# Optimization experiments

Measured on AMD Instinct MI355X. Metric: run time of the kernel, lower is better.

The kernel has to match this reference:

```python
import jax, jax.numpy as jnp
import numpy as np

B, LQ, LK, DIM = 2, 2048, 2048, 1024
HEADS, DH = 8, 64
INNER = HEADS * DH  # 512


def setup_inputs() -> dict:
    key = jax.random.key(0)
    ks = jax.random.split(key, 7)
    x = jax.random.normal(ks[0], (B, LQ, DIM), dtype=jnp.float32)
    y = jax.random.normal(ks[1], (B, LK, DIM), dtype=jnp.float32)
    # binary mask, 1 => masked (gets -1e9 added)
    mask = jax.random.randint(ks[2], (B, LQ, LK), 0, 2).astype(jnp.float32)
    s = 0.02
    Wq = jax.random.normal(ks[3], (INNER, DIM), dtype=jnp.float32) * s
    Wk = jax.random.normal(ks[4], (INNER, DIM), dtype=jnp.float32) * s
    Wv = jax.random.normal(ks[5], (INNER, DIM), dtype=jnp.float32) * s
    Wo = jax.random.normal(ks[6], (DIM, INNER), dtype=jnp.float32) * s
    return {"x": x, "y": y, "mask": mask, "Wq": Wq, "Wk": Wk, "Wv": Wv, "Wo": Wo}


def reference(x, y, mask, Wq, Wk, Wv, Wo):
    scale = DH ** -0.5
    # projections (Linear without bias: x @ W.T)
    q = (x @ Wq.T) * scale            # [B, LQ, INNER]
    k = y @ Wk.T                      # [B, LK, INNER]
    v = y @ Wv.T                      # [B, LK, INNER]
    # split into heads (torch.split along last dim == reshape to [.., H, DH])
    q = q.reshape(B, LQ, HEADS, DH)
    k = k.reshape(B, LK, HEADS, DH)
    v = v.reshape(B, LK, HEADS, DH)
    # per-head QK^T + additive mask*-1e9, softmax over keys, then V
    scores = jnp.einsum('bqhd,bkhd->bhqk', q, k) + mask[:, None, :, :] * (-1e9)
    attn = jax.nn.softmax(scores, axis=-1)
    out = jnp.einsum('bhqk,bkhd->bqhd', attn, v).reshape(B, LQ, INNER)
    return out @ Wo.T                 # [B, LQ, DIM]
```

## Files before the change

### kernel.cpp

```cpp
#include <hip/hip_runtime.h>
#include <hip/hip_bf16.h>
#include <stdint.h>

#define BATCH 2
#define LQ 2048
#define LK 2048
#define DIM 1024
#define HEADS 8
#define DH 64
#define INNER 512

typedef __attribute__((ext_vector_type(8))) short short8;
typedef __attribute__((ext_vector_type(4))) float f32x4;

__device__ __forceinline__ float bf2f(unsigned short u) {
    union { unsigned int i; float f; } v;
    v.i = ((unsigned int)u) << 16;
    return v.f;
}
__device__ __forceinline__ unsigned short f2bf(float f) {
    __hip_bfloat16 h = __float2bfloat16(f);
    return *reinterpret_cast<unsigned short*>(&h);
}
__device__ __forceinline__ void stc(unsigned short* C, size_t i, float v) { C[i] = f2bf(v); }
__device__ __forceinline__ void stc(float* C, size_t i, float v) { C[i] = v; }

typedef __attribute__((address_space(1))) const unsigned int gu32;
typedef __attribute__((address_space(3))) unsigned int lu32;
__device__ __forceinline__ void gload16(const void* g, void* l) {
    __builtin_amdgcn_global_load_lds((gu32*)g, (lu32*)l, 16, 0, 0);
}

__global__ __launch_bounds__(256) void cvt_all(
    const float* __restrict__ x,  const float* __restrict__ y,
    const float* __restrict__ wq, const float* __restrict__ wk,
    const float* __restrict__ wv, const float* __restrict__ wo,
    unsigned short* __restrict__ xb,  unsigned short* __restrict__ yb,
    unsigned short* __restrict__ wqb, unsigned short* __restrict__ wkb,
    unsigned short* __restrict__ wvb, unsigned short* __restrict__ wob)
{
    const float* src; unsigned short* dst; int n4;
    switch (blockIdx.y) {
        case 0: src = x;  dst = xb;  n4 = (BATCH * LQ * DIM) / 4; break;
        case 1: src = y;  dst = yb;  n4 = (BATCH * LK * DIM) / 4; break;
        case 2: src = wq; dst = wqb; n4 = (INNER * DIM) / 4; break;
        case 3: src = wk; dst = wkb; n4 = (INNER * DIM) / 4; break;
        case 4: src = wv; dst = wvb; n4 = (INNER * DIM) / 4; break;
        default: src = wo; dst = wob; n4 = (INNER * DIM) / 4; break;
    }
    const int stride = gridDim.x * 256;
    int i = blockIdx.x * 256 + threadIdx.x;
    for (; i + 3 * stride < n4; i += 4 * stride) {
        float4 f0 = ((const float4*)src)[i];
        float4 f1 = ((const float4*)src)[i + stride];
        float4 f2 = ((const float4*)src)[i + 2 * stride];
        float4 f3 = ((const float4*)src)[i + 3 * stride];
        ushort4 u0, u1, u2, u3;
        u0.x = f2bf(f0.x); u0.y = f2bf(f0.y); u0.z = f2bf(f0.z); u0.w = f2bf(f0.w);
        u1.x = f2bf(f1.x); u1.y = f2bf(f1.y); u1.z = f2bf(f1.z); u1.w = f2bf(f1.w);
        u2.x = f2bf(f2.x); u2.y = f2bf(f2.y); u2.z = f2bf(f2.z); u2.w = f2bf(f2.w);
        u3.x = f2bf(f3.x); u3.y = f2bf(f3.y); u3.z = f2bf(f3.z); u3.w = f2bf(f3.w);
        ((ushort4*)dst)[i] = u0;
        ((ushort4*)dst)[i + stride] = u1;
        ((ushort4*)dst)[i + 2 * stride] = u2;
        ((ushort4*)dst)[i + 3 * stride] = u3;
    }
    for (; i < n4; i += stride) {
        float4 f = ((const float4*)src)[i];
        ushort4 u;
        u.x = f2bf(f.x); u.y = f2bf(f.y); u.z = f2bf(f.z); u.w = f2bf(f.w);
        ((ushort4*)dst)[i] = u;
    }
}

__global__ __launch_bounds__(256) void pack_mask(
    const float* __restrict__ mask, unsigned long long* __restrict__ mbits)
{
    const int row = blockIdx.x * 4 + (threadIdx.x >> 6);
    const int lane = threadIdx.x & 63;
    const float* mp = mask + (size_t)row * LK;
    unsigned long long* ob = mbits + (size_t)row * (LK / 64);
#pragma unroll
    for (int c = 0; c < 32; c += 4) {
        float v0 = mp[(c + 0) * 64 + lane];
        float v1 = mp[(c + 1) * 64 + lane];
        float v2 = mp[(c + 2) * 64 + lane];
        float v3 = mp[(c + 3) * 64 + lane];
        unsigned long long b0 = __ballot(v0 > 0.5f);
        unsigned long long b1 = __ballot(v1 > 0.5f);
        unsigned long long b2 = __ballot(v2 > 0.5f);
        unsigned long long b3 = __ballot(v3 > 0.5f);
        if (lane == 0) { ob[c] = b0; ob[c + 1] = b1; ob[c + 2] = b2; ob[c + 3] = b3; }
    }
}

template <int IM, int JN, typename TC, int EPI>
__device__ __forceinline__ void gemm_body(
    const unsigned short* __restrict__ A,
    const unsigned short* __restrict__ W,
    TC* __restrict__ C,
    int K, int N, float scale,
    unsigned short* As, unsigned short* Bs)
{
    constexpr int BM = IM * 32;
    constexpr int BN = JN * 32;
    constexpr int ACH = BM * 8;
    constexpr int BCH = BN * 8;
    constexpr int AUS = BM * 64;
    constexpr int BUS = BN * 64;

    const int tid = threadIdx.x;
    const int m0 = blockIdx.x * BM;
    const int n0 = blockIdx.y * BN;
    const int w = tid >> 6, lane = tid & 63;
    const int q4 = lane >> 4, l16 = lane & 15;
    const int wm = (w >> 1) * (IM * 16), wn = (w & 1) * (JN * 16);
    const int sw = l16 & 7;

    f32x4 acc[IM][JN] = {};

#pragma unroll
    for (int i = 0; i < ACH / 256; ++i) {
        int s = tid + i * 256;
        int r = s >> 3, ch = (s & 7) ^ (r & 7);
        gload16(A + (size_t)(m0 + r) * K + ch * 8, As + (size_t)s * 8);
    }
#pragma unroll
    for (int i = 0; i < BCH / 256; ++i) {
        int s = tid + i * 256;
        int r = s >> 3, ch = (s & 7) ^ (r & 7);
        gload16(W + (size_t)(n0 + r) * K + ch * 8, Bs + (size_t)s * 8);
    }
    __syncthreads();

    const int nt = K / 64;
    for (int t = 0; t < nt; ++t) {
        const int curA = (t & 1) * AUS;
        const int curB = (t & 1) * BUS;
        if (t + 1 < nt) {
            int kk = (t + 1) * 64;
            const int nxtA = AUS - curA, nxtB = BUS - curB;
#pragma unroll
            for (int i = 0; i < ACH / 256; ++i) {
                int s = tid + i * 256;
                int r = s >> 3, ch = (s & 7) ^ (r & 7);
                gload16(A + (size_t)(m0 + r) * K + kk + ch * 8, As + nxtA + (size_t)s * 8);
            }
#pragma unroll
            for (int i = 0; i < BCH / 256; ++i) {
                int s = tid + i * 256;
                int r = s >> 3, ch = (s & 7) ^ (r & 7);
                gload16(W + (size_t)(n0 + r) * K + kk + ch * 8, Bs + nxtB + (size_t)s * 8);
            }
        }

#pragma unroll
        for (int ks = 0; ks < 2; ++ks) {
            const int kq = ((ks * 4 + q4) ^ sw) * 8;
            short8 a[IM], b[JN];
#pragma unroll
            for (int i = 0; i < IM; ++i)
                a[i] = *(const short8*)(As + curA + (wm + i * 16 + l16) * 64 + kq);
#pragma unroll
            for (int j = 0; j < JN; ++j)
                b[j] = *(const short8*)(Bs + curB + (wn + j * 16 + l16) * 64 + kq);
#pragma unroll
            for (int i = 0; i < IM; ++i)
#pragma unroll
                for (int j = 0; j < JN; ++j)
                    acc[i][j] = __builtin_amdgcn_mfma_f32_16x16x32_bf16(
                        a[i], b[j], acc[i][j], 0, 0, 0);
        }
        __syncthreads();
    }

    if (EPI == 0) {
#pragma unroll
        for (int i = 0; i < IM; ++i)
#pragma unroll
            for (int j = 0; j < JN; ++j)
#pragma unroll
                for (int r = 0; r < 4; ++r) {
                    int row = m0 + wm + i * 16 + q4 * 4 + r;
                    int col = n0 + wn + j * 16 + l16;
                    stc(C, (size_t)row * N + col, acc[i][j][r] * scale);
                }
    } else {
        constexpr int KW = IM * 16;
        constexpr int DW = JN * 16;
        constexpr int TPS = KW + 8;
        unsigned short* TP = As + w * (DW * TPS);
#pragma unroll
        for (int i = 0; i < IM; ++i)
#pragma unroll
            for (int j = 0; j < JN; ++j) {
                ushort4 u;
                u.x = f2bf(acc[i][j][0]); u.y = f2bf(acc[i][j][1]);
                u.z = f2bf(acc[i][j][2]); u.w = f2bf(acc[i][j][3]);
                *(ushort4*)(TP + (j * 16 + l16) * TPS + i * 16 + q4 * 4) = u;
            }
        const int keyflat = m0 + wm;
        const int bb = keyflat >> 11, key0 = keyflat & (LK - 1);
        const int hh = (n0 + wn) >> 6;
        const int dlow = (n0 + wn) & 63;
        constexpr int RCH = KW / 8;
        constexpr int NCH = DW * RCH;
#pragma unroll
        for (int p = 0; p < NCH / 64; ++p) {
            int c = p * 64 + lane;
            int dl = c / RCH, kc = c % RCH;
            uint4 v = *(const uint4*)(TP + dl * TPS + kc * 8);
            *(uint4*)((unsigned short*)C +
                ((size_t)((bb * HEADS + hh) * DH + dlow + dl)) * LK + key0 + kc * 8) = v;
        }
    }
}

__global__ __launch_bounds__(256) void proj_qkv(
    const unsigned short* __restrict__ xb, const unsigned short* __restrict__ yb,
    const unsigned short* __restrict__ wqb, const unsigned short* __restrict__ wkb,
    const unsigned short* __restrict__ wvb,
    unsigned short* __restrict__ qb, unsigned short* __restrict__ kb,
    unsigned short* __restrict__ vt)
{
    __shared__ __align__(16) unsigned short As[2 * 128 * 64];
    __shared__ __align__(16) unsigned short Bs[2 * 64 * 64];
    const int z = blockIdx.z;
    const unsigned short* A = (z == 0) ? xb : yb;
    const unsigned short* W = (z == 0) ? wqb : (z == 1) ? wkb : wvb;
    if (z == 2)
        gemm_body<4, 2, unsigned short, 1>(A, W, vt, DIM, INNER, 1.0f, As, Bs);
    else
        gemm_body<4, 2, unsigned short, 0>(A, W, (z == 0) ? qb : kb, DIM, INNER,
                                           (z == 0) ? 0.125f : 1.0f, As, Bs);
}

__global__ __launch_bounds__(256) void gemm_out(
    const unsigned short* __restrict__ A,
    const unsigned short* __restrict__ W,
    float* __restrict__ C)
{
    __shared__ __align__(16) unsigned short As[2 * 128 * 64];
    __shared__ __align__(16) unsigned short Bs[2 * 64 * 64];
    gemm_body<4, 2, float, 0>(A, W, C, INNER, DIM, 1.0f, As, Bs);
}

#define AT_US (64 * 64)

__global__ __launch_bounds__(256) void attn_mfma(
    const unsigned short* __restrict__ Q,
    const unsigned short* __restrict__ Kb,
    const unsigned short* __restrict__ Vt,
    const unsigned long long* __restrict__ Mb,
    unsigned short* __restrict__ O)
{
    __shared__ __align__(16) unsigned short Ks[2 * AT_US];
    __shared__ __align__(16) unsigned short Vs[2 * AT_US];
    __shared__ __align__(16) unsigned short Ps[4][16 * 72];

    const int tid = threadIdx.x;
    const int q0 = blockIdx.x * 64;
    const int h = blockIdx.y, b = blockIdx.z;
    const int w = tid >> 6, lane = tid & 63;
    const int q4 = lane >> 4, l16 = lane & 15;
    const int sw = l16 & 7;

    short8 qf[2];
    {
        const unsigned short* qp =
            Q + (size_t)(b * LQ + q0 + w * 16 + l16) * INNER + h * DH + q4 * 8;
        qf[0] = *(const short8*)(qp);
        qf[1] = *(const short8*)(qp + 32);
    }

    f32x4 o[4] = {};
    float lacc[4] = {0.f, 0.f, 0.f, 0.f};

    const unsigned short* kbase = Kb + (size_t)(b * LK) * INNER + h * DH;
    const unsigned short* vbase = Vt + (size_t)((b * HEADS + h) * DH) * LK;
    const unsigned long long* mrow =
        Mb + (size_t)(b * LQ + q0 + w * 16 + q4 * 4) * (LK / 64);

    const int r0 = tid >> 3, ch0 = (tid & 7) ^ (r0 & 7);
    const int s1 = tid + 256;
    const int r1 = s1 >> 3, ch1 = (s1 & 7) ^ (r1 & 7);

    gload16(kbase + (size_t)r0 * INNER + ch0 * 8, Ks + (size_t)tid * 8);
    gload16(kbase + (size_t)r1 * INNER + ch1 * 8, Ks + (size_t)s1 * 8);
    gload16(vbase + (size_t)r0 * LK + ch0 * 8, Vs + (size_t)tid * 8);
    gload16(vbase + (size_t)r1 * LK + ch1 * 8, Vs + (size_t)s1 * 8);
    __syncthreads();

    const int NT = LK / 64;
    for (int t = 0; t < NT; ++t) {
        const int cur = (t & 1) * AT_US;
        if (t + 1 < NT) {
            const int nxt = AT_US - cur;
            int kn = (t + 1) * 64;
            gload16(kbase + (size_t)(kn + r0) * INNER + ch0 * 8, Ks + nxt + (size_t)tid * 8);
            gload16(kbase + (size_t)(kn + r1) * INNER + ch1 * 8, Ks + nxt + (size_t)s1 * 8);
            gload16(vbase + (size_t)r0 * LK + kn + ch0 * 8, Vs + nxt + (size_t)tid * 8);
            gload16(vbase + (size_t)r1 * LK + kn + ch1 * 8, Vs + nxt + (size_t)s1 * 8);
        }

        f32x4 s[4];
#pragma unroll
        for (int j = 0; j < 4; ++j) {
            s[j] = f32x4{0.f, 0.f, 0.f, 0.f};
#pragma unroll
            for (int ks = 0; ks < 2; ++ks) {
                short8 kf = *(const short8*)(Ks + cur + (j * 16 + l16) * 64
                                             + (((ks * 4 + q4) ^ sw) * 8));
                s[j] = __builtin_amdgcn_mfma_f32_16x16x32_bf16(qf[ks], kf, s[j], 0, 0, 0);
            }
        }

#pragma unroll
        for (int r = 0; r < 4; ++r) {
            unsigned long long bits = mrow[(size_t)r * (LK / 64) + t];
#pragma unroll
            for (int j = 0; j < 4; ++j) {
                float e = __expf(s[j][r]);
                float pe = ((bits >> (j * 16 + l16)) & 1ull) ? 0.f : e;
                s[j][r] = pe;
                lacc[r] += pe;
            }
        }

#pragma unroll
        for (int j = 0; j < 4; ++j)
#pragma unroll
            for (int r = 0; r < 4; ++r)
                Ps[w][(q4 * 4 + r) * 72 + j * 16 + l16] = f2bf(s[j][r]);

#pragma unroll
        for (int ks = 0; ks < 2; ++ks) {
            short8 pf = *(const short8*)(&Ps[w][l16 * 72 + ks * 32 + q4 * 8]);
#pragma unroll
            for (int dd = 0; dd < 4; ++dd) {
                short8 vf = *(const short8*)(Vs + cur + (dd * 16 + l16) * 64
                                             + (((ks * 4 + q4) ^ sw) * 8));
                o[dd] = __builtin_amdgcn_mfma_f32_16x16x32_bf16(pf, vf, o[dd], 0, 0, 0);
            }
        }
        __syncthreads();
    }

#pragma unroll
    for (int off = 1; off < 16; off <<= 1)
#pragma unroll
        for (int r = 0; r < 4; ++r)
            lacc[r] += __shfl_xor(lacc[r], off);
    float inv[4];
#pragma unroll
    for (int r = 0; r < 4; ++r) inv[r] = 1.0f / lacc[r];

#pragma unroll
    for (int dd = 0; dd < 4; ++dd)
#pragma unroll
        for (int r = 0; r < 4; ++r) {
            int qrow = b * LQ + q0 + w * 16 + q4 * 4 + r;
            int col = h * DH + dd * 16 + l16;
            O[(size_t)qrow * INNER + col] = f2bf(o[dd][r] * inv[r]);
        }
}

extern "C" void kernel_launch(void* const* d_in, const int* in_sizes, int n_in,
                              void* d_out, int out_size, void* d_ws, size_t ws_size,
                              hipStream_t stream) {
    const float* x    = (const float*)d_in[0];
    const float* y    = (const float*)d_in[1];
    const float* mask = (const float*)d_in[2];
    const float* Wq   = (const float*)d_in[3];
    const float* Wk   = (const float*)d_in[4];
    const float* Wv   = (const float*)d_in[5];
    const float* Wo   = (const float*)d_in[6];
    float* out = (float*)d_out;

    const size_t NX = (size_t)BATCH * LQ * DIM;
    const size_t NS = (size_t)BATCH * LQ * INNER;
    const size_t NW = (size_t)INNER * DIM;
    unsigned short* xb  = (unsigned short*)d_ws;
    unsigned short* yb  = xb + NX;
    unsigned short* qb  = yb + NX;
    unsigned short* kb  = qb + NS;
    unsigned short* vt  = kb + NS;
    unsigned short* wqb = vt + NS;
    unsigned short* wkb = wqb + NW;
    unsigned short* wvb = wkb + NW;
    unsigned short* wob = wvb + NW;
    unsigned long long* mbits = (unsigned long long*)(wob + NW);
    unsigned short* ao  = xb;

    dim3 blk(256);
    cvt_all<<<dim3(256, 6), blk, 0, stream>>>(
        x, y, Wq, Wk, Wv, Wo, xb, yb, wqb, wkb, wvb, wob);
    pack_mask<<<dim3(BATCH * LQ / 4), blk, 0, stream>>>(mask, mbits);
    proj_qkv<<<dim3(4096 / 128, INNER / 64, 3), blk, 0, stream>>>(
        xb, yb, wqb, wkb, wvb, qb, kb, vt);
    attn_mfma<<<dim3(LQ / 64, HEADS, BATCH), blk, 0, stream>>>(
        qb, kb, vt, mbits, ao);
    gemm_out<<<dim3(4096 / 128, DIM / 64), blk, 0, stream>>>(ao, wob, out);
}
```

Before: 195.4 us.

## Fuse mask packing into conversion kernel, use packed bf16 converts and exp2 softmax

Merges the fp32-to-bf16 conversion and mask bit-packing into one prep launch with a larger grid, removing one kernel launch and letting both memory-bound passes overlap. Uses the packed two-value bf16 convert builtin where available, in the conversion loop, the V transpose epilogue and the P tile store. Folds log2(e) into the Q scale so the attention kernel can call exp2f instead of __expf. The conversion loop drops its manual 4x unroll, and grid-stride behaviour changes with the larger grid.

```diff
diff --git a/kernel.cpp b/kernel.cpp
--- a/kernel.cpp
+++ b/kernel.cpp
@@ -22,6 +22,16 @@
     __hip_bfloat16 h = __float2bfloat16(f);
     return *reinterpret_cast<unsigned short*>(&h);
 }
+__device__ __forceinline__ unsigned int f2bf2(float a, float b) {
+#if __has_builtin(__builtin_amdgcn_cvt_pk_bf16_f32)
+    typedef __attribute__((ext_vector_type(2))) __bf16 bf16x2;
+    union { bf16x2 v; unsigned int u; } cv;
+    cv.v = __builtin_amdgcn_cvt_pk_bf16_f32(a, b);
+    return cv.u;
+#else
+    return (unsigned int)f2bf(a) | ((unsigned int)f2bf(b) << 16);
+#endif
+}
 __device__ __forceinline__ void stc(unsigned short* C, size_t i, float v) { C[i] = f2bf(v); }
 __device__ __forceinline__ void stc(float* C, size_t i, float v) { C[i] = v; }
 
@@ -31,14 +41,35 @@
     __builtin_amdgcn_global_load_lds((gu32*)g, (lu32*)l, 16, 0, 0);
 }
 
-__global__ __launch_bounds__(256) void cvt_all(
+__global__ __launch_bounds__(256) void prep(
     const float* __restrict__ x,  const float* __restrict__ y,
     const float* __restrict__ wq, const float* __restrict__ wk,
     const float* __restrict__ wv, const float* __restrict__ wo,
+    const float* __restrict__ mask,
     unsigned short* __restrict__ xb,  unsigned short* __restrict__ yb,
     unsigned short* __restrict__ wqb, unsigned short* __restrict__ wkb,
-    unsigned short* __restrict__ wvb, unsigned short* __restrict__ wob)
+    unsigned short* __restrict__ wvb, unsigned short* __restrict__ wob,
+    unsigned long long* __restrict__ mbits)
 {
+    if (blockIdx.y == 6) {
+        const int wid = blockIdx.x * 4 + (threadIdx.x >> 6);
+        const int lane = threadIdx.x & 63;
+        for (int task = wid; task < BATCH * LQ * 8; task += 4096) {
+            int row = task >> 3, g = task & 7;
+            const float* mp = mask + (size_t)row * LK + g * 256;
+            unsigned long long* ob = mbits + (size_t)row * (LK / 64) + g * 4;
+            float v0 = mp[0 * 64 + lane];
+            float v1 = mp[1 * 64 + lane];
+            float v2 = mp[2 * 64 + lane];
+            float v3 = mp[3 * 64 + lane];
+            unsigned long long b0 = __ballot(v0 > 0.5f);
+            unsigned long long b1 = __ballot(v1 > 0.5f);
+            unsigned long long b2 = __ballot(v2 > 0.5f);
+            unsigned long long b3 = __ballot(v3 > 0.5f);
+            if (lane == 0) { ob[0] = b0; ob[1] = b1; ob[2] = b2; ob[3] = b3; }
+        }
+        return;
+    }
     const float* src; unsigned short* dst; int n4;
     switch (blockIdx.y) {
         case 0: src = x;  dst = xb;  n4 = (BATCH * LQ * DIM) / 4; break;
@@ -49,48 +80,12 @@
         default: src = wo; dst = wob; n4 = (INNER * DIM) / 4; break;
     }
     const int stride = gridDim.x * 256;
-    int i = blockIdx.x * 256 + threadIdx.x;
-    for (; i + 3 * stride < n4; i += 4 * stride) {
-        float4 f0 = ((const float4*)src)[i];
-        float4 f1 = ((const float4*)src)[i + stride];
-        float4 f2 = ((const float4*)src)[i + 2 * stride];
-        float4 f3 = ((const float4*)src)[i + 3 * stride];
-        ushort4 u0, u1, u2, u3;
-        u0.x = f2bf(f0.x); u0.y = f2bf(f0.y); u0.z = f2bf(f0.z); u0.w = f2bf(f0.w);
-        u1.x = f2bf(f1.x); u1.y = f2bf(f1.y); u1.z = f2bf(f1.z); u1.w = f2bf(f1.w);
-        u2.x = f2bf(f2.x); u2.y = f2bf(f2.y); u2.z = f2bf(f2.z); u2.w = f2bf(f2.w);
-        u3.x = f2bf(f3.x); u3.y = f2bf(f3.y); u3.z = f2bf(f3.z); u3.w = f2bf(f3.w);
-        ((ushort4*)dst)[i] = u0;
-        ((ushort4*)dst)[i + stride] = u1;
-        ((ushort4*)dst)[i + 2 * stride] = u2;
-        ((ushort4*)dst)[i + 3 * stride] = u3;
-    }
-    for (; i < n4; i += stride) {
+    for (int i = blockIdx.x * 256 + threadIdx.x; i < n4; i += stride) {
         float4 f = ((const float4*)src)[i];
         ushort4 u;
-        u.x = f2bf(f.x); u.y = f2bf(f.y); u.z = f2bf(f.z); u.w = f2bf(f.w);
+        unsigned int lo = f2bf2(f.x, f.y), hi = f2bf2(f.z, f.w);
+        u.x = lo & 0xffff; u.y = lo >> 16; u.z = hi & 0xffff; u.w = hi >> 16;
         ((ushort4*)dst)[i] = u;
-    }
-}
-
-__global__ __launch_bounds__(256) void pack_mask(
-    const float* __restrict__ mask, unsigned long long* __restrict__ mbits)
-{
-    const int row = blockIdx.x * 4 + (threadIdx.x >> 6);
-    const int lane = threadIdx.x & 63;
-    const float* mp = mask + (size_t)row * LK;
-    unsigned long long* ob = mbits + (size_t)row * (LK / 64);
-#pragma unroll
-    for (int c = 0; c < 32; c += 4) {
-        float v0 = mp[(c + 0) * 64 + lane];
-        float v1 = mp[(c + 1) * 64 + lane];
-        float v2 = mp[(c + 2) * 64 + lane];
-        float v3 = mp[(c + 3) * 64 + lane];
-        unsigned long long b0 = __ballot(v0 > 0.5f);
-        unsigned long long b1 = __ballot(v1 > 0.5f);
-        unsigned long long b2 = __ballot(v2 > 0.5f);
-        unsigned long long b3 = __ballot(v3 > 0.5f);
-        if (lane == 0) { ob[c] = b0; ob[c + 1] = b1; ob[c + 2] = b2; ob[c + 3] = b3; }
     }
 }
 
@@ -194,9 +189,10 @@
         for (int i = 0; i < IM; ++i)
 #pragma unroll
             for (int j = 0; j < JN; ++j) {
+                unsigned int lo = f2bf2(acc[i][j][0], acc[i][j][1]);
+                unsigned int hi = f2bf2(acc[i][j][2], acc[i][j][3]);
                 ushort4 u;
-                u.x = f2bf(acc[i][j][0]); u.y = f2bf(acc[i][j][1]);
-                u.z = f2bf(acc[i][j][2]); u.w = f2bf(acc[i][j][3]);
+                u.x = lo & 0xffff; u.y = lo >> 16; u.z = hi & 0xffff; u.w = hi >> 16;
                 *(ushort4*)(TP + (j * 16 + l16) * TPS + i * 16 + q4 * 4) = u;
             }
         const int keyflat = m0 + wm;
@@ -215,6 +211,8 @@
         }
     }
 }
+
+#define QSCALE 0.18033688011112042f
 
 __global__ __launch_bounds__(256) void proj_qkv(
     const unsigned short* __restrict__ xb, const unsigned short* __restrict__ yb,
@@ -232,7 +230,7 @@
         gemm_body<4, 2, unsigned short, 1>(A, W, vt, DIM, INNER, 1.0f, As, Bs);
     else
         gemm_body<4, 2, unsigned short, 0>(A, W, (z == 0) ? qb : kb, DIM, INNER,
-                                           (z == 0) ? 0.125f : 1.0f, As, Bs);
+                                           (z == 0) ? QSCALE : 1.0f, As, Bs);
 }
 
 __global__ __launch_bounds__(256) void gemm_out(
@@ -320,7 +318,7 @@
             unsigned long long bits = mrow[(size_t)r * (LK / 64) + t];
 #pragma unroll
             for (int j = 0; j < 4; ++j) {
-                float e = __expf(s[j][r]);
+                float e = exp2f(s[j][r]);
                 float pe = ((bits >> (j * 16 + l16)) & 1ull) ? 0.f : e;
                 s[j][r] = pe;
                 lacc[r] += pe;
@@ -328,10 +326,14 @@
         }
 
 #pragma unroll
-        for (int j = 0; j < 4; ++j)
-#pragma unroll
-            for (int r = 0; r < 4; ++r)
-                Ps[w][(q4 * 4 + r) * 72 + j * 16 + l16] = f2bf(s[j][r]);
+        for (int j = 0; j < 4; ++j) {
+            unsigned int lo = f2bf2(s[j][0], s[j][1]);
+            unsigned int hi = f2bf2(s[j][2], s[j][3]);
+            Ps[w][(q4 * 4 + 0) * 72 + j * 16 + l16] = lo & 0xffff;
+            Ps[w][(q4 * 4 + 1) * 72 + j * 16 + l16] = lo >> 16;
+            Ps[w][(q4 * 4 + 2) * 72 + j * 16 + l16] = hi & 0xffff;
+            Ps[w][(q4 * 4 + 3) * 72 + j * 16 + l16] = hi >> 16;
+        }
 
 #pragma unroll
         for (int ks = 0; ks < 2; ++ks) {
@@ -393,9 +395,8 @@
     unsigned short* ao  = xb;
 
     dim3 blk(256);
-    cvt_all<<<dim3(256, 6), blk, 0, stream>>>(
-        x, y, Wq, Wk, Wv, Wo, xb, yb, wqb, wkb, wvb, wob);
-    pack_mask<<<dim3(BATCH * LQ / 4), blk, 0, stream>>>(mask, mbits);
+    prep<<<dim3(1024, 7), blk, 0, stream>>>(
+        x, y, Wq, Wk, Wv, Wo, mask, xb, yb, wqb, wkb, wvb, wob, mbits);
     proj_qkv<<<dim3(4096 / 128, INNER / 64, 3), blk, 0, stream>>>(
         xb, yb, wqb, wkb, wvb, qb, kb, vt);
     attn_mfma<<<dim3(LQ / 64, HEADS, BATCH), blk, 0, stream>>>(
```

After: 204.5 us. +4.6%, slower.
